# Optimization experiments

Hardware: AMD Instinct MI355X
Metric: run time of the kernel (lower is better)

## Reference

```python
import jax, jax.numpy as jnp
import numpy as np

LAYERS = [2, 1024, 512, 256, 128, 1]
LB = jnp.array([0.0, 0.0], dtype=jnp.float32)
UB = jnp.array([2.0 * np.pi, 1.0], dtype=jnp.float32)


def _block_diag_mask(num_blocks, bs1, bs2):
    return jnp.kron(jnp.eye(num_blocks, dtype=jnp.float32), jnp.ones((bs1, bs2), jnp.float32))


def _masks():
    # masks for l in range(2, num_Layers - 2) with num_Layers = len(LAYERS) = 6 -> l in {2, 3}
    width = [LAYERS[0]] + [(2 ** (i - 1)) * LAYERS[i] for i in range(1, len(LAYERS) - 1)] + [LAYERS[-1]]
    masks = []
    for l in range(2, len(LAYERS) - 2):
        num_blocks = 2 ** (l - 1)
        bs1 = width[l] // num_blocks
        bs2 = 2 * LAYERS[l + 1]
        masks.append(_block_diag_mask(num_blocks, bs1, bs2))
    return masks


def setup_inputs() -> dict:
    key = jax.random.key(0)
    ks = jax.random.split(key, 8)
    N = 65536
    H = 1024

    def xavier(k, fi, fo):
        lim = float(np.sqrt(6.0 / (fi + fo)))
        return jax.random.uniform(k, (fi, fo), jnp.float32, -lim, lim)

    X = jax.random.uniform(ks[0], (N, 2), jnp.float32, 0.0, 1.0) * (UB - LB) + LB
    return {
        "X": X,
        "W0": xavier(ks[1], 2, H), "b0": jnp.zeros((1, H), jnp.float32),
        "W1": xavier(ks[2], H, H), "b1": jnp.zeros((1, H), jnp.float32),
        "W2": xavier(ks[3], H, H), "b2": jnp.zeros((1, H), jnp.float32),
        "W3": xavier(ks[4], H, H), "b3": jnp.zeros((1, H), jnp.float32),
        "W_last": xavier(ks[5], H, 1), "b_last": jnp.zeros((1, 1), jnp.float32),
    }


def reference(X, W0, b0, W1, b1, W2, b2, W3, b3, W_last, b_last):
    mask2, mask3 = _masks()
    # input normalization to [-1, 1]
    h = 2.0 * (X - LB) / (UB - LB) - 1.0
    h = jnp.tanh(h @ W0 + b0)                 # layer 0: dense
    h = jnp.tanh(h @ W1 + b1)                 # layer 1: dense (no mask in forward)
    h = jnp.tanh(h @ (W2 * mask2) + b2)       # layer 2: block-diagonal masked
    h = jnp.tanh(h @ (W3 * mask3) + b3)       # layer 3: block-diagonal masked
    return h @ W_last + b_last                # output layer, [N, 1]
```

## Files before the change

kernel.cpp:

```cpp
#include <hip/hip_runtime.h>
#include <cstdint>
#include <cstddef>


typedef _Float16  f16x8   __attribute__((ext_vector_type(8)));
typedef float     floatx4 __attribute__((ext_vector_type(4)));
typedef float     floatx8 __attribute__((ext_vector_type(8)));

__device__ __forceinline__ float tanh_fast(float x) {
    float e = __expf(2.0f * x);
    return 1.0f - 2.0f / (e + 1.0f);
}

__global__ __launch_bounds__(256)
void transposeH(const float* __restrict__ W, _Float16* __restrict__ Wt) {
    __shared__ float tile[32][33];
    const int tx = threadIdx.x & 31;
    const int ty = threadIdx.x >> 5;
    #pragma unroll
    for (int j = 0; j < 4; ++j) {
        int r = ty + j * 8;
        tile[r][tx] = W[(size_t)(blockIdx.y * 32 + r) * 1024 + blockIdx.x * 32 + tx];
    }
    __syncthreads();
    #pragma unroll
    for (int j = 0; j < 4; ++j) {
        int r = ty + j * 8;
        Wt[(size_t)(blockIdx.x * 32 + r) * 1024 + blockIdx.y * 32 + tx] =
            (_Float16)tile[tx][r];
    }
}

__global__ __launch_bounds__(256)
void init_out(float* __restrict__ out, const float* __restrict__ bl) {
    out[blockIdx.x * 256 + threadIdx.x] = bl[0];
}

__global__ __launch_bounds__(256)
void layer0_kernel(const float* __restrict__ X, const float* __restrict__ W0,
                   const float* __restrict__ b0, _Float16* __restrict__ H) {
    const int idx = blockIdx.x * 256 + threadIdx.x;
    const int row = idx >> 7;
    const int j0  = (idx & 127) << 3;
    const float x0 = X[row * 2 + 0];
    const float x1 = X[row * 2 + 1];
    const float xa = x0 * 0.31830988618379067f - 1.0f;
    const float xb = 2.0f * x1 - 1.0f;
    floatx8 wa = *(const floatx8*)(W0 + j0);
    floatx8 wb = *(const floatx8*)(W0 + 1024 + j0);
    floatx8 bb = *(const floatx8*)(b0 + j0);
    f16x8 o;
    #pragma unroll
    for (int j = 0; j < 8; ++j) {
        float v = fmaf(xa, wa[j], fmaf(xb, wb[j], bb[j]));
        o[j] = (_Float16)tanh_fast(v);
    }
    *(f16x8*)(H + (size_t)row * 1024 + j0) = o;
}

template <bool FUSE>
__global__ __launch_bounds__(512)
void gemm_tanh_f16(const _Float16* __restrict__ A, const _Float16* __restrict__ Bt,
                   const float* __restrict__ bias, _Float16* __restrict__ C,
                   const float* __restrict__ Wl, float* __restrict__ out, int KB) {
    __shared__ _Float16 As[256 * 32];
    __shared__ _Float16 Bs[128 * 32];

    const int tid  = threadIdx.x;
    const int lane = tid & 63;
    const int wave = tid >> 6;
    const int m0 = blockIdx.x * 256;
    const int n0 = blockIdx.y * 128;
    const int kbeg   = (n0 / KB) * KB;
    const int kiters = KB >> 5;
    const int wm = (wave & 3) << 6;
    const int wn = (wave >> 2) << 6;
    const int r = lane & 15;
    const int q = lane >> 4;

    const int rowA0 = tid >> 2;
    const int rowA1 = 128 + rowA0;
    const int seg   = (tid & 3) << 3;
    const size_t gA0 = (size_t)(m0 + rowA0) * 1024 + kbeg + seg;
    const size_t gA1 = (size_t)(m0 + rowA1) * 1024 + kbeg + seg;
    const size_t gB  = (size_t)(n0 + rowA0) * 1024 + kbeg + seg;
    const int ldsA0 = tid * 8;
    const int ldsA1 = (512 + tid) * 8;
    const int ldsB  = tid * 8;

    floatx4 acc[4][4];
    #pragma unroll
    for (int i = 0; i < 4; ++i)
        #pragma unroll
        for (int j = 0; j < 4; ++j)
            acc[i][j] = floatx4{0.f, 0.f, 0.f, 0.f};

    f16x8 va0 = *(const f16x8*)(A + gA0);
    f16x8 va1 = *(const f16x8*)(A + gA1);
    f16x8 vb  = *(const f16x8*)(Bt + gB);

    for (int t = 0; t < kiters; ++t) {
        __syncthreads();
        *(f16x8*)(As + ldsA0) = va0;
        *(f16x8*)(As + ldsA1) = va1;
        *(f16x8*)(Bs + ldsB)  = vb;
        __syncthreads();

        if (t + 1 < kiters) {
            const size_t d = (size_t)(t + 1) << 5;
            va0 = *(const f16x8*)(A + gA0 + d);
            va1 = *(const f16x8*)(A + gA1 + d);
            vb  = *(const f16x8*)(Bt + gB + d);
        }

        f16x8 af[4], bf[4];
        #pragma unroll
        for (int i = 0; i < 4; ++i) {
            af[i] = *(const f16x8*)(As + (wm + i * 16 + r) * 32 + q * 8);
            bf[i] = *(const f16x8*)(Bs + (wn + i * 16 + r) * 32 + q * 8);
        }
        #pragma unroll
        for (int i = 0; i < 4; ++i)
            #pragma unroll
            for (int j = 0; j < 4; ++j)
                acc[i][j] = __builtin_amdgcn_mfma_f32_16x16x32_f16(af[i], bf[j], acc[i][j], 0, 0, 0);
    }

    float bv[4], wlv[4];
    #pragma unroll
    for (int j = 0; j < 4; ++j) {
        const int col = n0 + wn + j * 16 + r;
        bv[j] = bias[col];
        if (FUSE) wlv[j] = Wl[col];
    }
    #pragma unroll
    for (int i = 0; i < 4; ++i) {
        const int row0 = m0 + wm + i * 16 + q * 4;
        #pragma unroll
        for (int rr = 0; rr < 4; ++rr) {
            if (!FUSE) {
                #pragma unroll
                for (int j = 0; j < 4; ++j) {
                    float o = tanh_fast(acc[i][j][rr] + bv[j]);
                    const int col = n0 + wn + j * 16 + r;
                    C[(size_t)(row0 + rr) * 1024 + col] = (_Float16)o;
                }
            } else {
                float p = 0.f;
                #pragma unroll
                for (int j = 0; j < 4; ++j)
                    p = fmaf(tanh_fast(acc[i][j][rr] + bv[j]), wlv[j], p);
                p += __shfl_down(p, 8);
                p += __shfl_down(p, 4);
                p += __shfl_down(p, 2);
                p += __shfl_down(p, 1);
                if (r == 0) atomicAdd(out + row0 + rr, p);
            }
        }
    }
}

extern "C" void kernel_launch(void* const* d_in, const int* in_sizes, int n_in,
                              void* d_out, int out_size, void* d_ws, size_t ws_size,
                              hipStream_t stream) {
    const float* X  = (const float*)d_in[0];
    const float* W0 = (const float*)d_in[1];
    const float* b0 = (const float*)d_in[2];
    const float* W1 = (const float*)d_in[3];
    const float* b1 = (const float*)d_in[4];
    const float* W2 = (const float*)d_in[5];
    const float* b2 = (const float*)d_in[6];
    const float* W3 = (const float*)d_in[7];
    const float* b3 = (const float*)d_in[8];
    const float* Wl = (const float*)d_in[9];
    const float* bl = (const float*)d_in[10];
    float* out = (float*)d_out;

    const int Nrows = in_sizes[0] / 2;
    const size_t WT = 1024 * 1024;
    const size_t wt_bytes = 3 * WT * 2;
    const size_t slack = 512;

    int R = 0;
    const int Rcap = Nrows < 32768 ? Nrows : 32768;
    for (int r = Rcap; r >= 256; r >>= 1)
        if ((size_t)2 * r * 2048 + wt_bytes + slack <= ws_size) { R = r; break; }
    if (!R) return;

    _Float16* wsp = (_Float16*)d_ws;
    _Float16* Wt1 = wsp;
    _Float16* Wt2 = Wt1 + WT;
    _Float16* Wt3 = Wt2 + WT;
    const size_t plane = (size_t)R * 1024;
    _Float16* P0 = Wt3 + WT;
    _Float16* P1 = P0 + plane;

    const dim3 tb(256);
    transposeH<<<dim3(32, 32), tb, 0, stream>>>(W1, Wt1);
    transposeH<<<dim3(32, 32), tb, 0, stream>>>(W2, Wt2);
    transposeH<<<dim3(32, 32), tb, 0, stream>>>(W3, Wt3);
    init_out<<<Nrows / 256, tb, 0, stream>>>(out, bl);

    const int nchunks = Nrows / R;
    for (int c = 0; c < nchunks; ++c) {
        const float* Xc = X + (size_t)c * R * 2;
        float* outc = out + (size_t)c * R;

        layer0_kernel<<<R / 2, tb, 0, stream>>>(Xc, W0, b0, P0);

        const dim3 tg(512);
        const dim3 gg(R / 256, 8);
        gemm_tanh_f16<false><<<gg, tg, 0, stream>>>(P0, Wt1, b1, P1, nullptr, nullptr, 1024);
        gemm_tanh_f16<false><<<gg, tg, 0, stream>>>(P1, Wt2, b2, P0, nullptr, nullptr, 512);
        gemm_tanh_f16<true ><<<gg, tg, 0, stream>>>(P0, Wt3, b3, nullptr, Wl, outc, 256);
    }
}
```

Measured before the change: 496.0 us.

## Add producer wave with double-buffered LDS to GEMM and merge transposes

The GEMM kernel is restructured into warp specialization. One dedicated loader wave streams A and B tiles from global memory into double-buffered LDS, while four compute waves issue MFMAs on 128x128 tiles. Block size drops from 512 to 320 threads with half the M tile, and the grid doubles. The three weight-transpose launches are merged into one 3D launch. The single loader wave must issue eight 16-byte loads per operand per k-step, which may become the bottleneck and leaves fewer compute waves per block.

```diff
diff --git a/kernel.cpp b/kernel.cpp
--- a/kernel.cpp
+++ b/kernel.cpp
@@ -13,7 +13,11 @@
 }
 
 __global__ __launch_bounds__(256)
-void transposeH(const float* __restrict__ W, _Float16* __restrict__ Wt) {
+void transposeH3(const float* __restrict__ W1, const float* __restrict__ W2,
+                 const float* __restrict__ W3, _Float16* __restrict__ Wt1,
+                 _Float16* __restrict__ Wt2, _Float16* __restrict__ Wt3) {
+    const float* W = blockIdx.z == 0 ? W1 : (blockIdx.z == 1 ? W2 : W3);
+    _Float16* Wt   = blockIdx.z == 0 ? Wt1 : (blockIdx.z == 1 ? Wt2 : Wt3);
     __shared__ float tile[32][33];
     const int tx = threadIdx.x & 31;
     const int ty = threadIdx.x >> 5;
@@ -59,35 +63,63 @@
 }
 
 template <bool FUSE>
-__global__ __launch_bounds__(512)
+__global__ __launch_bounds__(320)
 void gemm_tanh_f16(const _Float16* __restrict__ A, const _Float16* __restrict__ Bt,
                    const float* __restrict__ bias, _Float16* __restrict__ C,
                    const float* __restrict__ Wl, float* __restrict__ out, int KB) {
-    __shared__ _Float16 As[256 * 32];
-    __shared__ _Float16 Bs[128 * 32];
+    __shared__ _Float16 lds[2][8192];
 
     const int tid  = threadIdx.x;
     const int lane = tid & 63;
     const int wave = tid >> 6;
-    const int m0 = blockIdx.x * 256;
+    const int m0 = blockIdx.x * 128;
     const int n0 = blockIdx.y * 128;
     const int kbeg   = (n0 / KB) * KB;
     const int kiters = KB >> 5;
-    const int wm = (wave & 3) << 6;
-    const int wn = (wave >> 2) << 6;
+
+    if (wave == 4) {
+        const int row0 = lane >> 2;
+        const int sg   = (lane & 3) << 3;
+        const size_t gaBase = (size_t)(m0 + row0) * 1024 + kbeg + sg;
+        const size_t gbBase = (size_t)(n0 + row0) * 1024 + kbeg + sg;
+        const int lsBase = lane * 8;
+        f16x8 ra[8], rb[8];
+        #pragma unroll
+        for (int i = 0; i < 8; ++i) {
+            ra[i] = *(const f16x8*)(A + gaBase + (size_t)i * 16384);
+            rb[i] = *(const f16x8*)(Bt + gbBase + (size_t)i * 16384);
+        }
+        #pragma unroll
+        for (int i = 0; i < 8; ++i) {
+            *(f16x8*)(&lds[0][lsBase + i * 512]) = ra[i];
+            *(f16x8*)(&lds[0][4096 + lsBase + i * 512]) = rb[i];
+        }
+        __syncthreads();
+        for (int t = 0; t < kiters; ++t) {
+            if (t + 1 < kiters) {
+                const size_t d = (size_t)(t + 1) << 5;
+                #pragma unroll
+                for (int i = 0; i < 8; ++i) {
+                    ra[i] = *(const f16x8*)(A + gaBase + (size_t)i * 16384 + d);
+                    rb[i] = *(const f16x8*)(Bt + gbBase + (size_t)i * 16384 + d);
+                }
+                _Float16* dst = lds[(t + 1) & 1];
+                #pragma unroll
+                for (int i = 0; i < 8; ++i) {
+                    *(f16x8*)(dst + lsBase + i * 512) = ra[i];
+                    *(f16x8*)(dst + 4096 + lsBase + i * 512) = rb[i];
+                }
+            }
+            __syncthreads();
+        }
+        return;
+    }
+
+    const int wm = (wave & 1) << 6;
+    const int wn = (wave >> 1) << 6;
     const int r = lane & 15;
     const int q = lane >> 4;
 
-    const int rowA0 = tid >> 2;
-    const int rowA1 = 128 + rowA0;
-    const int seg   = (tid & 3) << 3;
-    const size_t gA0 = (size_t)(m0 + rowA0) * 1024 + kbeg + seg;
-    const size_t gA1 = (size_t)(m0 + rowA1) * 1024 + kbeg + seg;
-    const size_t gB  = (size_t)(n0 + rowA0) * 1024 + kbeg + seg;
-    const int ldsA0 = tid * 8;
-    const int ldsA1 = (512 + tid) * 8;
-    const int ldsB  = tid * 8;
-
     floatx4 acc[4][4];
     #pragma unroll
     for (int i = 0; i < 4; ++i)
@@ -95,24 +127,10 @@
         for (int j = 0; j < 4; ++j)
             acc[i][j] = floatx4{0.f, 0.f, 0.f, 0.f};
 
-    f16x8 va0 = *(const f16x8*)(A + gA0);
-    f16x8 va1 = *(const f16x8*)(A + gA1);
-    f16x8 vb  = *(const f16x8*)(Bt + gB);
-
+    __syncthreads();
     for (int t = 0; t < kiters; ++t) {
-        __syncthreads();
-        *(f16x8*)(As + ldsA0) = va0;
-        *(f16x8*)(As + ldsA1) = va1;
-        *(f16x8*)(Bs + ldsB)  = vb;
-        __syncthreads();
-
-        if (t + 1 < kiters) {
-            const size_t d = (size_t)(t + 1) << 5;
-            va0 = *(const f16x8*)(A + gA0 + d);
-            va1 = *(const f16x8*)(A + gA1 + d);
-            vb  = *(const f16x8*)(Bt + gB + d);
-        }
-
+        const _Float16* As = lds[t & 1];
+        const _Float16* Bs = As + 4096;
         f16x8 af[4], bf[4];
         #pragma unroll
         for (int i = 0; i < 4; ++i) {
@@ -124,6 +142,7 @@
             #pragma unroll
             for (int j = 0; j < 4; ++j)
                 acc[i][j] = __builtin_amdgcn_mfma_f32_16x16x32_f16(af[i], bf[j], acc[i][j], 0, 0, 0);
+        __syncthreads();
     }
 
     float bv[4], wlv[4];
@@ -196,9 +215,7 @@
     _Float16* P1 = P0 + plane;
 
     const dim3 tb(256);
-    transposeH<<<dim3(32, 32), tb, 0, stream>>>(W1, Wt1);
-    transposeH<<<dim3(32, 32), tb, 0, stream>>>(W2, Wt2);
-    transposeH<<<dim3(32, 32), tb, 0, stream>>>(W3, Wt3);
+    transposeH3<<<dim3(32, 32, 3), tb, 0, stream>>>(W1, W2, W3, Wt1, Wt2, Wt3);
     init_out<<<Nrows / 256, tb, 0, stream>>>(out, bl);
 
     const int nchunks = Nrows / R;
@@ -208,8 +225,8 @@
 
         layer0_kernel<<<R / 2, tb, 0, stream>>>(Xc, W0, b0, P0);
 
-        const dim3 tg(512);
-        const dim3 gg(R / 256, 8);
+        const dim3 tg(320);
+        const dim3 gg(R / 128, 8);
         gemm_tanh_f16<false><<<gg, tg, 0, stream>>>(P0, Wt1, b1, P1, nullptr, nullptr, 1024);
         gemm_tanh_f16<false><<<gg, tg, 0, stream>>>(P1, Wt2, b2, P0, nullptr, nullptr, 512);
         gemm_tanh_f16<true ><<<gg, tg, 0, stream>>>(P0, Wt3, b3, nullptr, Wl, outc, 256);
```

After: 584.5 us. 17.8% more time.

## Load GEMM B fragments directly to registers and shrink tile to 128x128

Applied to the files above, without the earlier changes.

The GEMM block shrinks from 512 threads with a 256x128 tile to 256 threads with a 128x128 tile. Each wave now loads its B (weight) MFMA fragments straight from global memory into registers, double-buffered across k-steps, and the B shared-memory tile is dropped. This cuts LDS traffic and shared-memory footprint, and the smaller blocks should give more concurrent blocks per CU. In exchange, B fragments are no longer shared across waves through LDS, so redundant global/L2 reads of the weights rise, and register pressure grows. The three weight transposes are also merged into one launch.

```diff
diff --git a/kernel.cpp b/kernel.cpp
--- a/kernel.cpp
+++ b/kernel.cpp
@@ -13,7 +13,11 @@
 }
 
 __global__ __launch_bounds__(256)
-void transposeH(const float* __restrict__ W, _Float16* __restrict__ Wt) {
+void transposeH3(const float* __restrict__ W1, const float* __restrict__ W2,
+                 const float* __restrict__ W3, _Float16* __restrict__ Wt1,
+                 _Float16* __restrict__ Wt2, _Float16* __restrict__ Wt3) {
+    const float* W = blockIdx.z == 0 ? W1 : (blockIdx.z == 1 ? W2 : W3);
+    _Float16* Wt   = blockIdx.z == 0 ? Wt1 : (blockIdx.z == 1 ? Wt2 : Wt3);
     __shared__ float tile[32][33];
     const int tx = threadIdx.x & 31;
     const int ty = threadIdx.x >> 5;
@@ -59,34 +63,32 @@
 }
 
 template <bool FUSE>
-__global__ __launch_bounds__(512)
+__global__ __launch_bounds__(256)
 void gemm_tanh_f16(const _Float16* __restrict__ A, const _Float16* __restrict__ Bt,
                    const float* __restrict__ bias, _Float16* __restrict__ C,
                    const float* __restrict__ Wl, float* __restrict__ out, int KB) {
-    __shared__ _Float16 As[256 * 32];
-    __shared__ _Float16 Bs[128 * 32];
+    __shared__ _Float16 As[128 * 32];
 
     const int tid  = threadIdx.x;
     const int lane = tid & 63;
     const int wave = tid >> 6;
-    const int m0 = blockIdx.x * 256;
+    const int m0 = blockIdx.x * 128;
     const int n0 = blockIdx.y * 128;
     const int kbeg   = (n0 / KB) * KB;
     const int kiters = KB >> 5;
-    const int wm = (wave & 3) << 6;
-    const int wn = (wave >> 2) << 6;
+    const int wm = (wave & 1) << 6;
+    const int wn = (wave >> 1) << 6;
     const int r = lane & 15;
     const int q = lane >> 4;
 
-    const int rowA0 = tid >> 2;
-    const int rowA1 = 128 + rowA0;
-    const int seg   = (tid & 3) << 3;
-    const size_t gA0 = (size_t)(m0 + rowA0) * 1024 + kbeg + seg;
-    const size_t gA1 = (size_t)(m0 + rowA1) * 1024 + kbeg + seg;
-    const size_t gB  = (size_t)(n0 + rowA0) * 1024 + kbeg + seg;
+    const int rowS = tid >> 2;
+    const int seg  = (tid & 3) << 3;
+    const size_t gA0 = (size_t)(m0 + rowS) * 1024 + kbeg + seg;
+    const size_t gA1 = gA0 + (size_t)64 * 1024;
     const int ldsA0 = tid * 8;
-    const int ldsA1 = (512 + tid) * 8;
-    const int ldsB  = tid * 8;
+    const int ldsA1 = (256 + tid) * 8;
+
+    const size_t gB = (size_t)(n0 + wn + r) * 1024 + kbeg + q * 8;
 
     floatx4 acc[4][4];
     #pragma unroll
@@ -97,33 +99,38 @@
 
     f16x8 va0 = *(const f16x8*)(A + gA0);
     f16x8 va1 = *(const f16x8*)(A + gA1);
-    f16x8 vb  = *(const f16x8*)(Bt + gB);
+    f16x8 bc[4], bn[4];
+    #pragma unroll
+    for (int j = 0; j < 4; ++j)
+        bc[j] = *(const f16x8*)(Bt + gB + (size_t)j * 16384);
 
     for (int t = 0; t < kiters; ++t) {
         __syncthreads();
         *(f16x8*)(As + ldsA0) = va0;
         *(f16x8*)(As + ldsA1) = va1;
-        *(f16x8*)(Bs + ldsB)  = vb;
         __syncthreads();
 
         if (t + 1 < kiters) {
             const size_t d = (size_t)(t + 1) << 5;
             va0 = *(const f16x8*)(A + gA0 + d);
             va1 = *(const f16x8*)(A + gA1 + d);
-            vb  = *(const f16x8*)(Bt + gB + d);
+            #pragma unroll
+            for (int j = 0; j < 4; ++j)
+                bn[j] = *(const f16x8*)(Bt + gB + (size_t)j * 16384 + d);
         }
 
-        f16x8 af[4], bf[4];
-        #pragma unroll
-        for (int i = 0; i < 4; ++i) {
+        f16x8 af[4];
+        #pragma unroll
+        for (int i = 0; i < 4; ++i)
             af[i] = *(const f16x8*)(As + (wm + i * 16 + r) * 32 + q * 8);
-            bf[i] = *(const f16x8*)(Bs + (wn + i * 16 + r) * 32 + q * 8);
-        }
         #pragma unroll
         for (int i = 0; i < 4; ++i)
             #pragma unroll
             for (int j = 0; j < 4; ++j)
-                acc[i][j] = __builtin_amdgcn_mfma_f32_16x16x32_f16(af[i], bf[j], acc[i][j], 0, 0, 0);
+                acc[i][j] = __builtin_amdgcn_mfma_f32_16x16x32_f16(af[i], bc[j], acc[i][j], 0, 0, 0);
+        #pragma unroll
+        for (int j = 0; j < 4; ++j)
+            bc[j] = bn[j];
     }
 
     float bv[4], wlv[4];
@@ -196,9 +203,7 @@
     _Float16* P1 = P0 + plane;
 
     const dim3 tb(256);
-    transposeH<<<dim3(32, 32), tb, 0, stream>>>(W1, Wt1);
-    transposeH<<<dim3(32, 32), tb, 0, stream>>>(W2, Wt2);
-    transposeH<<<dim3(32, 32), tb, 0, stream>>>(W3, Wt3);
+    transposeH3<<<dim3(32, 32, 3), tb, 0, stream>>>(W1, W2, W3, Wt1, Wt2, Wt3);
     init_out<<<Nrows / 256, tb, 0, stream>>>(out, bl);
 
     const int nchunks = Nrows / R;
@@ -208,10 +213,9 @@
 
         layer0_kernel<<<R / 2, tb, 0, stream>>>(Xc, W0, b0, P0);
 
-        const dim3 tg(512);
-        const dim3 gg(R / 256, 8);
-        gemm_tanh_f16<false><<<gg, tg, 0, stream>>>(P0, Wt1, b1, P1, nullptr, nullptr, 1024);
-        gemm_tanh_f16<false><<<gg, tg, 0, stream>>>(P1, Wt2, b2, P0, nullptr, nullptr, 512);
-        gemm_tanh_f16<true ><<<gg, tg, 0, stream>>>(P0, Wt3, b3, nullptr, Wl, outc, 256);
-    }
-}
+        const dim3 gg(R / 128, 8);
+        gemm_tanh_f16<false><<<gg, tb, 0, stream>>>(P0, Wt1, b1, P1, nullptr, nullptr, 1024);
+        gemm_tanh_f16<false><<<gg, tb, 0, stream>>>(P1, Wt2, b2, P0, nullptr, nullptr, 512);
+        gemm_tanh_f16<true ><<<gg, tb, 0, stream>>>(P0, Wt3, b3, nullptr, Wl, outc, 256);
+    }
+}
```

Result: slower. 676.7 us (+36.4%).

## Double GEMM K-tile to 64 and merge weight transposes with output init

Applied to the files above, without the earlier changes.

The GEMM kernel now stages a 64-wide K slice per iteration instead of 32, so each tile load and pair of barriers feeds two rounds of MFMA work, and the global loads are rearranged into 8 lanes per row. This halves the number of barrier-separated iterations, at the cost of double the LDS per block, which may lower occupancy. The three weight-transpose launches and the output-init launch are also merged into one 3D-grid launch to cut launch overhead. The merged kernel's init slice covers 32*32*256 entries guarded by the row count.

```diff
diff --git a/kernel.cpp b/kernel.cpp
--- a/kernel.cpp
+++ b/kernel.cpp
@@ -13,7 +13,18 @@
 }
 
 __global__ __launch_bounds__(256)
-void transposeH(const float* __restrict__ W, _Float16* __restrict__ Wt) {
+void transposeH3(const float* __restrict__ W1, const float* __restrict__ W2,
+                 const float* __restrict__ W3, _Float16* __restrict__ Wt1,
+                 _Float16* __restrict__ Wt2, _Float16* __restrict__ Wt3,
+                 float* __restrict__ out, const float* __restrict__ bl,
+                 int nrows) {
+    if (blockIdx.z == 3) {
+        const int id = (blockIdx.y * 32 + blockIdx.x) * 256 + threadIdx.x;
+        if (id * 1 < nrows) out[id] = bl[0];
+        return;
+    }
+    const float* W = blockIdx.z == 0 ? W1 : (blockIdx.z == 1 ? W2 : W3);
+    _Float16* Wt   = blockIdx.z == 0 ? Wt1 : (blockIdx.z == 1 ? Wt2 : Wt3);
     __shared__ float tile[32][33];
     const int tx = threadIdx.x & 31;
     const int ty = threadIdx.x >> 5;
@@ -29,11 +40,6 @@
         Wt[(size_t)(blockIdx.x * 32 + r) * 1024 + blockIdx.y * 32 + tx] =
             (_Float16)tile[tx][r];
     }
-}
-
-__global__ __launch_bounds__(256)
-void init_out(float* __restrict__ out, const float* __restrict__ bl) {
-    out[blockIdx.x * 256 + threadIdx.x] = bl[0];
 }
 
 __global__ __launch_bounds__(256)
@@ -63,8 +69,8 @@
 void gemm_tanh_f16(const _Float16* __restrict__ A, const _Float16* __restrict__ Bt,
                    const float* __restrict__ bias, _Float16* __restrict__ C,
                    const float* __restrict__ Wl, float* __restrict__ out, int KB) {
-    __shared__ _Float16 As[256 * 32];
-    __shared__ _Float16 Bs[128 * 32];
+    __shared__ _Float16 As[256 * 64];
+    __shared__ _Float16 Bs[128 * 64];
 
     const int tid  = threadIdx.x;
     const int lane = tid & 63;
@@ -72,21 +78,17 @@
     const int m0 = blockIdx.x * 256;
     const int n0 = blockIdx.y * 128;
     const int kbeg   = (n0 / KB) * KB;
-    const int kiters = KB >> 5;
+    const int kiters = KB >> 6;
     const int wm = (wave & 3) << 6;
     const int wn = (wave >> 2) << 6;
     const int r = lane & 15;
     const int q = lane >> 4;
 
-    const int rowA0 = tid >> 2;
-    const int rowA1 = 128 + rowA0;
-    const int seg   = (tid & 3) << 3;
-    const size_t gA0 = (size_t)(m0 + rowA0) * 1024 + kbeg + seg;
-    const size_t gA1 = (size_t)(m0 + rowA1) * 1024 + kbeg + seg;
-    const size_t gB  = (size_t)(n0 + rowA0) * 1024 + kbeg + seg;
-    const int ldsA0 = tid * 8;
-    const int ldsA1 = (512 + tid) * 8;
-    const int ldsB  = tid * 8;
+    const int rowS = tid >> 3;
+    const int segS = (tid & 7) << 3;
+    const size_t gA = (size_t)(m0 + rowS) * 1024 + kbeg + segS;
+    const size_t gB = (size_t)(n0 + rowS) * 1024 + kbeg + segS;
+    const int ldsS = tid * 8;
 
     floatx4 acc[4][4];
     #pragma unroll
@@ -95,35 +97,42 @@
         for (int j = 0; j < 4; ++j)
             acc[i][j] = floatx4{0.f, 0.f, 0.f, 0.f};
 
-    f16x8 va0 = *(const f16x8*)(A + gA0);
-    f16x8 va1 = *(const f16x8*)(A + gA1);
-    f16x8 vb  = *(const f16x8*)(Bt + gB);
+    f16x8 va[4], vb[2];
+    #pragma unroll
+    for (int i = 0; i < 4; ++i) va[i] = *(const f16x8*)(A + gA + (size_t)i * 65536);
+    #pragma unroll
+    for (int i = 0; i < 2; ++i) vb[i] = *(const f16x8*)(Bt + gB + (size_t)i * 65536);
 
     for (int t = 0; t < kiters; ++t) {
         __syncthreads();
-        *(f16x8*)(As + ldsA0) = va0;
-        *(f16x8*)(As + ldsA1) = va1;
-        *(f16x8*)(Bs + ldsB)  = vb;
+        #pragma unroll
+        for (int i = 0; i < 4; ++i) *(f16x8*)(As + ldsS + i * 4096) = va[i];
+        #pragma unroll
+        for (int i = 0; i < 2; ++i) *(f16x8*)(Bs + ldsS + i * 4096) = vb[i];
         __syncthreads();
 
         if (t + 1 < kiters) {
-            const size_t d = (size_t)(t + 1) << 5;
-            va0 = *(const f16x8*)(A + gA0 + d);
-            va1 = *(const f16x8*)(A + gA1 + d);
-            vb  = *(const f16x8*)(Bt + gB + d);
+            const size_t d = (size_t)(t + 1) << 6;
+            #pragma unroll
+            for (int i = 0; i < 4; ++i) va[i] = *(const f16x8*)(A + gA + (size_t)i * 65536 + d);
+            #pragma unroll
+            for (int i = 0; i < 2; ++i) vb[i] = *(const f16x8*)(Bt + gB + (size_t)i * 65536 + d);
         }
 
-        f16x8 af[4], bf[4];
-        #pragma unroll
-        for (int i = 0; i < 4; ++i) {
-            af[i] = *(const f16x8*)(As + (wm + i * 16 + r) * 32 + q * 8);
-            bf[i] = *(const f16x8*)(Bs + (wn + i * 16 + r) * 32 + q * 8);
+        #pragma unroll
+        for (int sub = 0; sub < 2; ++sub) {
+            f16x8 af[4], bf[4];
+            #pragma unroll
+            for (int i = 0; i < 4; ++i) {
+                af[i] = *(const f16x8*)(As + (wm + i * 16 + r) * 64 + sub * 32 + q * 8);
+                bf[i] = *(const f16x8*)(Bs + (wn + i * 16 + r) * 64 + sub * 32 + q * 8);
+            }
+            #pragma unroll
+            for (int i = 0; i < 4; ++i)
+                #pragma unroll
+                for (int j = 0; j < 4; ++j)
+                    acc[i][j] = __builtin_amdgcn_mfma_f32_16x16x32_f16(af[i], bf[j], acc[i][j], 0, 0, 0);
         }
-        #pragma unroll
-        for (int i = 0; i < 4; ++i)
-            #pragma unroll
-            for (int j = 0; j < 4; ++j)
-                acc[i][j] = __builtin_amdgcn_mfma_f32_16x16x32_f16(af[i], bf[j], acc[i][j], 0, 0, 0);
     }
 
     float bv[4], wlv[4];
@@ -196,10 +205,8 @@
     _Float16* P1 = P0 + plane;
 
     const dim3 tb(256);
-    transposeH<<<dim3(32, 32), tb, 0, stream>>>(W1, Wt1);
-    transposeH<<<dim3(32, 32), tb, 0, stream>>>(W2, Wt2);
-    transposeH<<<dim3(32, 32), tb, 0, stream>>>(W3, Wt3);
-    init_out<<<Nrows / 256, tb, 0, stream>>>(out, bl);
+    transposeH3<<<dim3(32, 32, 4), tb, 0, stream>>>(W1, W2, W3, Wt1, Wt2, Wt3,
+                                                    out, bl, Nrows);
 
     const int nchunks = Nrows / R;
     for (int c = 0; c < nchunks; ++c) {
```

New measurement: 591.4 us. 19.2% more time.
